# Kernel tuning notes

Hardware: AMD Instinct MI355X
Metric: run time of the kernel (lower is better)

Reference implementation:

```python
import jax, jax.numpy as jnp
import numpy as np
import math

B, S, D, H = 4, 2048, 512, 8
HD = D // H

def setup_inputs() -> dict:
    key = jax.random.key(0)
    ks = jax.random.split(key, 12)
    s_hd = 1.0 / math.sqrt(HD)
    s_d = 1.0 / math.sqrt(D)
    return {
        "q": jax.random.normal(ks[0], (B, S, D), jnp.float32),
        "k": jax.random.normal(ks[1], (B, S, D), jnp.float32),
        "v": jax.random.normal(ks[2], (B, S, D), jnp.float32),
        # torch nn.Linear(head_dim, head_dim): weight [HD, HD], bias [HD]
        "Wq": jax.random.uniform(ks[3], (HD, HD), jnp.float32, -s_hd, s_hd),
        "bq": jax.random.uniform(ks[4], (HD,), jnp.float32, -s_hd, s_hd),
        "Wk": jax.random.uniform(ks[5], (HD, HD), jnp.float32, -s_hd, s_hd),
        "bk": jax.random.uniform(ks[6], (HD,), jnp.float32, -s_hd, s_hd),
        "Wv": jax.random.uniform(ks[7], (HD, HD), jnp.float32, -s_hd, s_hd),
        "bv": jax.random.uniform(ks[8], (HD,), jnp.float32, -s_hd, s_hd),
        # output projection nn.Linear(d, d)
        "Wo": jax.random.uniform(ks[9], (D, D), jnp.float32, -s_d, s_d),
        "bo": jax.random.uniform(ks[10], (D,), jnp.float32, -s_d, s_d),
        # LayerNorm(d) affine params
        "gamma": jnp.ones((D,), jnp.float32),
        "beta": jnp.zeros((D,), jnp.float32),
    }

def _layernorm(x, gamma, beta, eps=1e-5):
    mu = jnp.mean(x, axis=-1, keepdims=True)
    var = jnp.var(x, axis=-1, keepdims=True)
    return (x - mu) * jax.lax.rsqrt(var + eps) * gamma + beta

def reference(q, k, v, Wq, bq, Wk, bk, Wv, bv, Wo, bo, gamma, beta):
    batch, q_len = q.shape[0], q.shape[1]
    # split heads: [B, L, H, HD]; per-head Linear shares one weight across heads
    Qh = q.reshape(batch, q_len, H, HD) @ Wq.T + bq
    Kh = k.reshape(batch, k.shape[1], H, HD) @ Wk.T + bk
    Vh = v.reshape(batch, v.shape[1], H, HD) @ Wv.T + bv
    # scores scaled by sqrt(d) (faithful to source, NOT sqrt(head_dim))
    scores = jnp.einsum('bqhd,bkhd->bhqk', Qh, Kh) / math.sqrt(D)
    attn = jax.nn.softmax(scores, axis=-1)
    out = jnp.einsum('bhqk,bkhd->bqhd', attn, Vh)
    concat = out.reshape(batch, q_len, D)
    lin = concat @ Wo.T + bo
    # AddNorm quirk: residual added AFTER LayerNorm (dropout = identity in eval)
    return q + _layernorm(lin, gamma, beta)
```

## Files before the change

kernel.cpp:

```cpp
#include <hip/hip_runtime.h>
#include <hip/hip_bf16.h>
#include <math.h>
#include <stdint.h>

#define B 4
#define S 2048
#define D 512
#define H 8
#define HD 64

typedef __attribute__((ext_vector_type(4))) int   int4v;
typedef __attribute__((ext_vector_type(8))) short short8;
typedef __attribute__((ext_vector_type(4))) short short4v;
typedef __attribute__((ext_vector_type(4))) float f32x4;

__device__ __forceinline__ unsigned short bfr(float x) {
    __bf16 h = (__bf16)x;
    union { __bf16 b; unsigned short s; } u; u.b = h; return u.s;
}
__device__ __forceinline__ float b2f(unsigned short s) {
    union { unsigned u; float f; } v; v.u = (unsigned)s << 16; return v.f;
}
__device__ __forceinline__ float ex2(float x) {
#if __has_builtin(__builtin_amdgcn_exp2f)
    return __builtin_amdgcn_exp2f(x);
#else
    return exp2f(x);
#endif
}
__device__ __forceinline__ short8 cvt8(const float* p) {
    float4 f0 = *(const float4*)p;
    float4 f1 = *(const float4*)(p + 4);
    short8 s8;
    s8[0] = (short)bfr(f0.x); s8[1] = (short)bfr(f0.y);
    s8[2] = (short)bfr(f0.z); s8[3] = (short)bfr(f0.w);
    s8[4] = (short)bfr(f1.x); s8[5] = (short)bfr(f1.y);
    s8[6] = (short)bfr(f1.z); s8[7] = (short)bfr(f1.w);
    return s8;
}

#define QSCALE 0.06377229601488305f
#define MFIX 4.0f

typedef const __attribute__((address_space(1))) unsigned char g8_t;
typedef __attribute__((address_space(3))) unsigned char l8_t;
__device__ __forceinline__ void gl_lds16(const unsigned short* g, unsigned short* l) {
#if __has_builtin(__builtin_amdgcn_global_load_lds)
    __builtin_amdgcn_global_load_lds((g8_t*)g, (l8_t*)l, 16, 0, 0);
#else
    int lane = threadIdx.x & 63;
    ((int4v*)l)[lane] = *(const int4v*)g;
#endif
}

__global__ __launch_bounds__(256) void qkv_mfma_kernel(
    const float* __restrict__ q, const float* __restrict__ k,
    const float* __restrict__ v,
    const float* __restrict__ Wq, const float* __restrict__ bq,
    const float* __restrict__ Wk, const float* __restrict__ bk,
    const float* __restrict__ Wv, const float* __restrict__ bv,
    const float* __restrict__ Wo, unsigned short* __restrict__ WoB,
    unsigned short* __restrict__ Qh, unsigned short* __restrict__ Kh,
    unsigned short* __restrict__ VtG)
{
    const int t = threadIdx.x;
    const int bid = blockIdx.x;
    if (bid >= 1536) {
        int i = (bid - 1536) * 1024 + t * 4;
        float4 f = *(const float4*)(Wo + i);
        short4v s;
        s[0] = (short)bfr(f.x); s[1] = (short)bfr(f.y);
        s[2] = (short)bfr(f.z); s[3] = (short)bfr(f.w);
        *(short4v*)(WoB + i) = s;
        return;
    }

    __shared__ __align__(16) unsigned short Wl[64 * 72];

    const int x   = bid / 512;
    const int r_  = bid - x * 512;
    const int bh  = r_ >> 4;
    const int stg = r_ & 15;
    const int b = bh >> 3, h = bh & 7;
    const int L = t & 63, w = t >> 6;
    const int c = L & 15, qd = L >> 4;

    const float* Wf     = (x == 0) ? Wq : (x == 1) ? Wk : Wv;
    const float* bias_p = (x == 0) ? bq : (x == 1) ? bk : bv;
    const float* X      = (x == 0) ? q  : (x == 1) ? k  : v;

    {
        int row = t >> 2, col = (t & 3) * 16;
        *(short8*)&Wl[row * 72 + col]     = cvt8(Wf + t * 16);
        *(short8*)&Wl[row * 72 + col + 8] = cvt8(Wf + t * 16 + 8);
    }
    __syncthreads();

    short8 wf[4][2];
    #pragma unroll
    for (int nt = 0; nt < 4; ++nt)
        #pragma unroll
        for (int kc = 0; kc < 2; ++kc)
            wf[nt][kc] = *(const short8*)&Wl[(16 * nt + c) * 72 + kc * 32 + 8 * qd];

    if (x < 2) {
        float bias[4];
        #pragma unroll
        for (int nt = 0; nt < 4; ++nt) bias[nt] = bias_p[16 * nt + c];
        const float sc = (x == 0) ? QSCALE : 1.0f;
        #pragma unroll
        for (int ti = 0; ti < 2; ++ti) {
            const int st = stg * 8 + w * 2 + ti;
            const float* xrow = X + ((size_t)(b * S + st * 16 + c)) * D + h * HD;
            short8 af0 = cvt8(xrow + 8 * qd);
            short8 af1 = cvt8(xrow + 32 + 8 * qd);
            f32x4 acc[4];
            #pragma unroll
            for (int nt = 0; nt < 4; ++nt) {
                acc[nt] = (f32x4){bias[nt], bias[nt], bias[nt], bias[nt]};
                acc[nt] = __builtin_amdgcn_mfma_f32_16x16x32_bf16(af0, wf[nt][0], acc[nt], 0, 0, 0);
                acc[nt] = __builtin_amdgcn_mfma_f32_16x16x32_bf16(af1, wf[nt][1], acc[nt], 0, 0, 0);
            }
            unsigned short* O = ((x == 0) ? Qh : Kh)
                              + ((size_t)(b * H + h) * S + st * 16) * HD;
            #pragma unroll
            for (int nt = 0; nt < 4; ++nt)
                #pragma unroll
                for (int r = 0; r < 4; ++r)
                    O[(4 * qd + r) * HD + 16 * nt + c] = bfr(acc[nt][r] * sc);
        }
    } else {
        f32x4 bias4[4];
        #pragma unroll
        for (int nt = 0; nt < 4; ++nt) {
            float4 bb4 = *(const float4*)(bias_p + 16 * nt + 4 * qd);
            bias4[nt] = (f32x4){bb4.x, bb4.y, bb4.z, bb4.w};
        }
        #pragma unroll
        for (int ti = 0; ti < 2; ++ti) {
            const int st = stg * 8 + w * 2 + ti;
            const float* xrow = X + ((size_t)(b * S + st * 16 + c)) * D + h * HD;
            short8 af0 = cvt8(xrow + 8 * qd);
            short8 af1 = cvt8(xrow + 32 + 8 * qd);
            f32x4 acc[4];
            #pragma unroll
            for (int nt = 0; nt < 4; ++nt) {
                acc[nt] = bias4[nt];
                acc[nt] = __builtin_amdgcn_mfma_f32_16x16x32_bf16(wf[nt][0], af0, acc[nt], 0, 0, 0);
                acc[nt] = __builtin_amdgcn_mfma_f32_16x16x32_bf16(wf[nt][1], af1, acc[nt], 0, 0, 0);
            }
            unsigned short* O = VtG + (size_t)(b * H + h) * HD * S;
            #pragma unroll
            for (int nt = 0; nt < 4; ++nt)
                #pragma unroll
                for (int r = 0; r < 4; ++r)
                    O[(size_t)(16 * nt + 4 * qd + r) * S + st * 16 + c] = bfr(acc[nt][r]);
        }
    }
}

__global__ __launch_bounds__(256, 4) void attn_kernel(
    const unsigned short* __restrict__ Qh, const unsigned short* __restrict__ Kh,
    const unsigned short* __restrict__ VtG, unsigned short* __restrict__ accPb,
    float* __restrict__ lP)
{
    __shared__ __align__(16) unsigned short Ks[2][4096];
    __shared__ __align__(16) unsigned short Vs[2][4096];

    const int idx = blockIdx.x;
    const int bh = idx & 31;
    const int rem = idx >> 5;
    const int qt = rem >> 1;
    const int ks = rem & 1;
    const int b = bh >> 3, h = bh & 7;
    const int t = threadIdx.x;
    const int w = t >> 6, L = t & 63;
    const int c = L & 15, qd = L >> 4;

    const unsigned short* Kb = Kh + ((size_t)bh * S + ks * 1024) * HD;
    const unsigned short* Vb = VtG + (size_t)bh * HD * S + ks * 1024;

    short8 qf[2][2];
    #pragma unroll
    for (int qg = 0; qg < 2; ++qg)
        #pragma unroll
        for (int kc = 0; kc < 2; ++kc)
            qf[qg][kc] = *(const short8*)(Qh
                + ((size_t)bh * S + qt * 128 + w * 32 + qg * 16 + c) * HD
                + kc * 32 + 8 * qd);

    f32x4 acc[2][4];
    float lrun[2] = {0.f, 0.f};
    #pragma unroll
    for (int qg = 0; qg < 2; ++qg)
        #pragma unroll
        for (int dt = 0; dt < 4; ++dt) acc[qg][dt] = (f32x4){0.f, 0.f, 0.f, 0.f};

    const int sd = t >> 3, sj = t & 7;
    const int sp = sj >> 2, smt = (sj >> 1) & 1;
    const int sqa = (2 * sj) & 3, sqb = (2 * sj + 1) & 3;

    int4v vpre[2];
    #pragma unroll
    for (int i = 0; i < 2; ++i) {
        int bi = w + 4 * i;
        gl_lds16(Kb + (size_t)(16 * (bi >> 1) + c) * HD + (bi & 1) * 32 + qd * 8,
                 &Ks[0][bi * 512]);
        vpre[i] = *(const int4v*)(Vb + (size_t)(sd + 32 * i) * S + 8 * sj);
    }

    for (int it = 0; it < 16; ++it) {
        const int cur = it & 1, nxt = cur ^ 1;
        #pragma unroll
        for (int i = 0; i < 2; ++i) {
            int d = sd + 32 * i;
            int dt = d >> 4, cc = d & 15;
            union { int4v v; short4v h[2]; } u; u.v = vpre[i];
            *(short4v*)&Vs[cur][((dt * 2 + sp) * 64 + sqa * 16 + cc) * 8 + smt * 4] = u.h[0];
            *(short4v*)&Vs[cur][((dt * 2 + sp) * 64 + sqb * 16 + cc) * 8 + smt * 4] = u.h[1];
        }
        __syncthreads();
        if (it + 1 < 16) {
            int n1 = (it + 1) * 64;
            #pragma unroll
            for (int i = 0; i < 2; ++i) {
                int bi = w + 4 * i;
                gl_lds16(Kb + (size_t)(n1 + 16 * (bi >> 1) + c) * HD + (bi & 1) * 32 + qd * 8,
                         &Ks[nxt][bi * 512]);
                vpre[i] = *(const int4v*)(Vb + (size_t)(sd + 32 * i) * S + n1 + 8 * sj);
            }
        }

        const unsigned short* KsC = Ks[cur];
        const unsigned short* VsC = Vs[cur];

        short4v pa[2][4];
        #pragma unroll
        for (int mt = 0; mt < 4; ++mt) {
            short8 a0 = *(const short8*)(KsC + (mt * 2 + 0) * 512 + L * 8);
            short8 a1 = *(const short8*)(KsC + (mt * 2 + 1) * 512 + L * 8);
            #pragma unroll
            for (int qg = 0; qg < 2; ++qg) {
                f32x4 stv = (f32x4){-MFIX, -MFIX, -MFIX, -MFIX};
                __builtin_amdgcn_s_setprio(1);
                stv = __builtin_amdgcn_mfma_f32_16x16x32_bf16(a0, qf[qg][0], stv, 0, 0, 0);
                stv = __builtin_amdgcn_mfma_f32_16x16x32_bf16(a1, qf[qg][1], stv, 0, 0, 0);
                __builtin_amdgcn_s_setprio(0);
                float p0 = ex2(stv[0]), p1 = ex2(stv[1]);
                float p2 = ex2(stv[2]), p3 = ex2(stv[3]);
                lrun[qg] += (p0 + p1) + (p2 + p3);
                short4v p_;
                p_[0] = (short)bfr(p0); p_[1] = (short)bfr(p1);
                p_[2] = (short)bfr(p2); p_[3] = (short)bfr(p3);
                pa[qg][mt] = p_;
            }
        }

        #pragma unroll
        for (int dt = 0; dt < 4; ++dt)
            #pragma unroll
            for (int p = 0; p < 2; ++p) {
                union { short8 v8; short4v h[2]; } u;
                u.v8 = *(const short8*)(VsC + (dt * 2 + p) * 512 + L * 8);
#if __has_builtin(__builtin_amdgcn_mfma_f32_16x16x16bf16_1k)
                __builtin_amdgcn_s_setprio(1);
                #pragma unroll
                for (int qg = 0; qg < 2; ++qg) {
                    acc[qg][dt] = __builtin_amdgcn_mfma_f32_16x16x16bf16_1k(
                        pa[qg][2 * p + 0], u.h[0], acc[qg][dt], 0, 0, 0);
                    acc[qg][dt] = __builtin_amdgcn_mfma_f32_16x16x16bf16_1k(
                        pa[qg][2 * p + 1], u.h[1], acc[qg][dt], 0, 0, 0);
                }
                __builtin_amdgcn_s_setprio(0);
#else
                __builtin_amdgcn_s_setprio(1);
                #pragma unroll
                for (int qg = 0; qg < 2; ++qg) {
                    short8 pz0 = {pa[qg][2 * p + 0][0], pa[qg][2 * p + 0][1],
                                  pa[qg][2 * p + 0][2], pa[qg][2 * p + 0][3], 0, 0, 0, 0};
                    short8 pz1 = {pa[qg][2 * p + 1][0], pa[qg][2 * p + 1][1],
                                  pa[qg][2 * p + 1][2], pa[qg][2 * p + 1][3], 0, 0, 0, 0};
                    short8 v0 = {u.h[0][0], u.h[0][1], u.h[0][2], u.h[0][3], 0, 0, 0, 0};
                    short8 v1 = {u.h[1][0], u.h[1][1], u.h[1][2], u.h[1][3], 0, 0, 0, 0};
                    acc[qg][dt] = __builtin_amdgcn_mfma_f32_16x16x32_bf16(pz0, v0, acc[qg][dt], 0, 0, 0);
                    acc[qg][dt] = __builtin_amdgcn_mfma_f32_16x16x32_bf16(pz1, v1, acc[qg][dt], 0, 0, 0);
                }
                __builtin_amdgcn_s_setprio(0);
#endif
            }
    }

    const int q0 = qt * 128 + w * 32;
    unsigned short* accPp = accPb + (size_t)ks * ((size_t)B * S * D)
                          + ((size_t)b * S + q0) * D + h * HD;
    #pragma unroll
    for (int qg = 0; qg < 2; ++qg) {
        float lr = lrun[qg];
        lr += __shfl_xor(lr, 16);
        lr += __shfl_xor(lr, 32);
        if (qd == 0)
            lP[(size_t)ks * ((size_t)B * H * S) + (size_t)bh * S + q0 + qg * 16 + c] = lr;
        #pragma unroll
        for (int dt = 0; dt < 4; ++dt)
            #pragma unroll
            for (int r = 0; r < 4; ++r)
                accPp[(size_t)(qg * 16 + 4 * qd + r) * D + 16 * dt + c]
                    = bfr(acc[qg][dt][r]);
    }
}

__global__ __launch_bounds__(1024) void oproj_ln_kernel(
    const unsigned short* __restrict__ accPb, const float* __restrict__ lP,
    const unsigned short* __restrict__ WoB,
    const float* __restrict__ bo, const float* __restrict__ gamma,
    const float* __restrict__ beta, const float* __restrict__ qin,
    float* __restrict__ out)
{
    __shared__ __align__(16) unsigned short As[32 * 520];
    __shared__ float red[2][32][17];
    __shared__ float linv_s[32][8];
    __shared__ float mu_s2[32], rs_s2[32];

    const int t = threadIdx.x;
    const int r0 = blockIdx.x * 32;
    const int w = t >> 6, L = t & 63;
    const int c = L & 15, qd = L >> 4;
    const int n0 = w * 32;
    const size_t NEh = (size_t)B * S * D;
    const size_t BHS = (size_t)B * H * S;

    if (t < 256) {
        int row = t >> 3, hh = t & 7;
        int bb = r0 >> 11;
        int ss = (r0 & (S - 1)) + row;
        float l0 = lP[(size_t)(bb * H + hh) * S + ss];
        float l1 = lP[BHS + (size_t)(bb * H + hh) * S + ss];
        linv_s[row][hh] = 1.f / (l0 + l1);
    }
    __syncthreads();

    #pragma unroll
    for (int i = 0; i < 4; ++i) {
        int flat = t + 1024 * i;
        int row = flat >> 7, cg4 = flat & 127;
        int col = cg4 * 4;
        size_t gi = (size_t)(r0 + row) * D + col;
        short4v a0 = *(const short4v*)(accPb + gi);
        short4v a1 = *(const short4v*)(accPb + NEh + gi);
        float li = linv_s[row][col >> 6];
        short4v s;
        #pragma unroll
        for (int j = 0; j < 4; ++j)
            s[j] = (short)bfr((b2f((unsigned short)a0[j])
                             + b2f((unsigned short)a1[j])) * li);
        *(short4v*)&As[row * 520 + col] = s;
    }
    __syncthreads();

    f32x4 acc[2][2];
    #pragma unroll
    for (int nt = 0; nt < 2; ++nt) {
        float bv_ = bo[n0 + 16 * nt + c];
        acc[0][nt] = (f32x4){bv_, bv_, bv_, bv_};
        acc[1][nt] = (f32x4){bv_, bv_, bv_, bv_};
    }

    for (int kc = 0; kc < 16; ++kc) {
        short8 a0 = *(const short8*)&As[c * 520 + kc * 32 + 8 * qd];
        short8 a1 = *(const short8*)&As[(16 + c) * 520 + kc * 32 + 8 * qd];
        #pragma unroll
        for (int nt = 0; nt < 2; ++nt) {
            short8 bf = *(const short8*)(WoB + (size_t)(n0 + 16 * nt + c) * D
                                         + kc * 32 + 8 * qd);
            acc[0][nt] = __builtin_amdgcn_mfma_f32_16x16x32_bf16(a0, bf, acc[0][nt], 0, 0, 0);
            acc[1][nt] = __builtin_amdgcn_mfma_f32_16x16x32_bf16(a1, bf, acc[1][nt], 0, 0, 0);
        }
    }

    float sm[2][4], sq[2][4];
    #pragma unroll
    for (int mt = 0; mt < 2; ++mt)
        #pragma unroll
        for (int r = 0; r < 4; ++r) { sm[mt][r] = 0.f; sq[mt][r] = 0.f; }
    #pragma unroll
    for (int mt = 0; mt < 2; ++mt)
        #pragma unroll
        for (int nt = 0; nt < 2; ++nt)
            #pragma unroll
            for (int r = 0; r < 4; ++r) {
                float x_ = acc[mt][nt][r];
                sm[mt][r] += x_; sq[mt][r] += x_ * x_;
            }
    #pragma unroll
    for (int mask = 1; mask <= 8; mask <<= 1)
        #pragma unroll
        for (int mt = 0; mt < 2; ++mt)
            #pragma unroll
            for (int r = 0; r < 4; ++r) {
                sm[mt][r] += __shfl_xor(sm[mt][r], mask);
                sq[mt][r] += __shfl_xor(sq[mt][r], mask);
            }
    if (c == 0) {
        #pragma unroll
        for (int mt = 0; mt < 2; ++mt)
            #pragma unroll
            for (int r = 0; r < 4; ++r) {
                red[0][mt * 16 + 4 * qd + r][w] = sm[mt][r];
                red[1][mt * 16 + 4 * qd + r][w] = sq[mt][r];
            }
    }
    __syncthreads();

    if (t < 32) {
        float s_ = 0.f, q_ = 0.f;
        #pragma unroll
        for (int w_ = 0; w_ < 16; ++w_) { s_ += red[0][t][w_]; q_ += red[1][t][w_]; }
        float mu_ = s_ * (1.f / D);
        float var = q_ * (1.f / D) - mu_ * mu_;
        mu_s2[t] = mu_;
        rs_s2[t] = rsqrtf(var + 1e-5f);
    }
    __syncthreads();

    #pragma unroll
    for (int nt = 0; nt < 2; ++nt) {
        int n = n0 + 16 * nt + c;
        float g = gamma[n], be = beta[n];
        #pragma unroll
        for (int mt = 0; mt < 2; ++mt)
            #pragma unroll
            for (int r = 0; r < 4; ++r) {
                int m = mt * 16 + 4 * qd + r;
                size_t gi = (size_t)(r0 + m) * D + n;
                out[gi] = qin[gi] + (acc[mt][nt][r] - mu_s2[m]) * rs_s2[m] * g + be;
            }
    }
}

extern "C" void kernel_launch(void* const* d_in, const int* in_sizes, int n_in,
                              void* d_out, int out_size, void* d_ws, size_t ws_size,
                              hipStream_t stream) {
    const float* q     = (const float*)d_in[0];
    const float* k     = (const float*)d_in[1];
    const float* v     = (const float*)d_in[2];
    const float* Wq    = (const float*)d_in[3];
    const float* bq    = (const float*)d_in[4];
    const float* Wk    = (const float*)d_in[5];
    const float* bk    = (const float*)d_in[6];
    const float* Wv    = (const float*)d_in[7];
    const float* bv    = (const float*)d_in[8];
    const float* Wo    = (const float*)d_in[9];
    const float* bo    = (const float*)d_in[10];
    const float* gamma = (const float*)d_in[11];
    const float* beta  = (const float*)d_in[12];
    float* out = (float*)d_out;

    const size_t NE = (size_t)B * S * D;
    unsigned short* wsu = (unsigned short*)d_ws;
    unsigned short* Qh    = wsu;
    unsigned short* Kh    = wsu + NE;
    unsigned short* VtG   = wsu + 2 * NE;
    unsigned short* WoB   = wsu + 3 * NE;
    unsigned short* accPb = WoB + (size_t)D * D;
    float* lP = (float*)(accPb + 2 * NE);

    hipLaunchKernelGGL(qkv_mfma_kernel, dim3(1536 + 256), dim3(256), 0, stream,
                       q, k, v, Wq, bq, Wk, bk, Wv, bv, Wo, WoB, Qh, Kh, VtG);
    hipLaunchKernelGGL(attn_kernel, dim3(1024), dim3(256), 0, stream,
                       Qh, Kh, VtG, accPb, lP);
    hipLaunchKernelGGL(oproj_ln_kernel, dim3(B * S / 32), dim3(1024), 0, stream,
                       accPb, lP, WoB, bo, gamma, beta, q, out);
}
```

Baseline: 194.1 us.

## Stage projection outputs through LDS for coalesced stores; swizzle V tile layout

The QKV projection kernel now writes its MFMA results into a per-wave LDS scratch tile and reads them back as 16-byte rows, so Qh/Kh and the transposed V output go out as vectorized, coalesced global stores instead of scattered 2-byte writes. In the attention kernel, the V shared-memory tile gets an XOR swizzle on both the write and read addresses to reduce LDS bank conflicts. This adds some LDS traffic and extra shared memory per block in the projection kernel.

```diff
diff --git a/kernel.cpp b/kernel.cpp
--- a/kernel.cpp
+++ b/kernel.cpp
@@ -76,6 +76,7 @@
     }
 
     __shared__ __align__(16) unsigned short Wl[64 * 72];
+    __shared__ __align__(16) unsigned short Tb[4][1536];
 
     const int x   = bid / 512;
     const int r_  = bid - x * 512;
@@ -89,6 +90,8 @@
     const float* bias_p = (x == 0) ? bq : (x == 1) ? bk : bv;
     const float* X      = (x == 0) ? q  : (x == 1) ? k  : v;
 
+    unsigned short* Tw = Tb[w];
+
     {
         int row = t >> 2, col = (t & 3) * 16;
         *(short8*)&Wl[row * 72 + col]     = cvt8(Wf + t * 16);
@@ -121,13 +124,18 @@
                 acc[nt] = __builtin_amdgcn_mfma_f32_16x16x32_bf16(af0, wf[nt][0], acc[nt], 0, 0, 0);
                 acc[nt] = __builtin_amdgcn_mfma_f32_16x16x32_bf16(af1, wf[nt][1], acc[nt], 0, 0, 0);
             }
-            unsigned short* O = ((x == 0) ? Qh : Kh)
-                              + ((size_t)(b * H + h) * S + st * 16) * HD;
             #pragma unroll
             for (int nt = 0; nt < 4; ++nt)
                 #pragma unroll
                 for (int r = 0; r < 4; ++r)
-                    O[(4 * qd + r) * HD + 16 * nt + c] = bfr(acc[nt][r] * sc);
+                    Tw[(4 * qd + r) * 72 + 16 * nt + c] = bfr(acc[nt][r] * sc);
+            int rw = L >> 2, cg_ = (L & 3) * 16;
+            short8 s0 = *(const short8*)&Tw[rw * 72 + cg_];
+            short8 s1 = *(const short8*)&Tw[rw * 72 + cg_ + 8];
+            unsigned short* O = ((x == 0) ? Qh : Kh)
+                              + ((size_t)(b * H + h) * S + st * 16) * HD;
+            *(short8*)&O[rw * HD + cg_]     = s0;
+            *(short8*)&O[rw * HD + cg_ + 8] = s1;
         }
     } else {
         f32x4 bias4[4];
@@ -149,12 +157,16 @@
                 acc[nt] = __builtin_amdgcn_mfma_f32_16x16x32_bf16(wf[nt][0], af0, acc[nt], 0, 0, 0);
                 acc[nt] = __builtin_amdgcn_mfma_f32_16x16x32_bf16(wf[nt][1], af1, acc[nt], 0, 0, 0);
             }
-            unsigned short* O = VtG + (size_t)(b * H + h) * HD * S;
             #pragma unroll
             for (int nt = 0; nt < 4; ++nt)
                 #pragma unroll
                 for (int r = 0; r < 4; ++r)
-                    O[(size_t)(16 * nt + 4 * qd + r) * S + st * 16 + c] = bfr(acc[nt][r]);
+                    Tw[(16 * nt + 4 * qd + r) * 24 + c] = bfr(acc[nt][r]);
+            short8 s0 = *(const short8*)&Tw[L * 24];
+            short8 s1 = *(const short8*)&Tw[L * 24 + 8];
+            unsigned short* O = VtG + (size_t)(b * H + h) * HD * S;
+            *(short8*)&O[(size_t)L * S + st * 16]     = s0;
+            *(short8*)&O[(size_t)L * S + st * 16 + 8] = s1;
         }
     }
 }
@@ -199,6 +211,8 @@
     const int sd = t >> 3, sj = t & 7;
     const int sp = sj >> 2, smt = (sj >> 1) & 1;
     const int sqa = (2 * sj) & 3, sqb = (2 * sj + 1) & 3;
+    int voff0 = (((0 * 2 + sp) * 64 + sqa * 16 + 0) * 8 + smt * 4) * 2;
+    int voff1 = (((0 * 2 + sp) * 64 + sqb * 16 + 0) * 8 + smt * 4) * 2;
 
     int4v vpre[2];
     #pragma unroll
@@ -211,13 +225,18 @@
 
     for (int it = 0; it < 16; ++it) {
         const int cur = it & 1, nxt = cur ^ 1;
+        unsigned char* VsB = (unsigned char*)&Vs[cur][0];
         #pragma unroll
         for (int i = 0; i < 2; ++i) {
             int d = sd + 32 * i;
             int dt = d >> 4, cc = d & 15;
             union { int4v v; short4v h[2]; } u; u.v = vpre[i];
-            *(short4v*)&Vs[cur][((dt * 2 + sp) * 64 + sqa * 16 + cc) * 8 + smt * 4] = u.h[0];
-            *(short4v*)&Vs[cur][((dt * 2 + sp) * 64 + sqb * 16 + cc) * 8 + smt * 4] = u.h[1];
+            int o0 = voff0 + dt * 2048 + cc * 16;
+            int o1 = voff1 + dt * 2048 + cc * 16;
+            o0 ^= ((o0 >> 8) & 3) << 5;
+            o1 ^= ((o1 >> 8) & 3) << 5;
+            *(short4v*)(VsB + o0) = u.h[0];
+            *(short4v*)(VsB + o1) = u.h[1];
         }
         __syncthreads();
         if (it + 1 < 16) {
@@ -232,7 +251,7 @@
         }
 
         const unsigned short* KsC = Ks[cur];
-        const unsigned short* VsC = Vs[cur];
+        const unsigned char* VsR = (const unsigned char*)&Vs[cur][0];
 
         short4v pa[2][4];
         #pragma unroll
@@ -260,8 +279,10 @@
         for (int dt = 0; dt < 4; ++dt)
             #pragma unroll
             for (int p = 0; p < 2; ++p) {
+                int roff = ((dt * 2 + p) * 512 + L * 8) * 2;
+                roff ^= ((roff >> 8) & 3) << 5;
                 union { short8 v8; short4v h[2]; } u;
-                u.v8 = *(const short8*)(VsC + (dt * 2 + p) * 512 + L * 8);
+                u.v8 = *(const short8*)(VsR + roff);
 #if __has_builtin(__builtin_amdgcn_mfma_f32_16x16x16bf16_1k)
                 __builtin_amdgcn_s_setprio(1);
                 #pragma unroll
```

Result: no change. 192.7 us (-0.8%).
